# Kernel optimization log

Hardware: AMD Instinct MI355X
Metric: run time of the kernel (lower is better)

The kernel has to match this reference:

```python
import jax, jax.numpy as jnp
import numpy as np

H = 1024      # lstm_hidden_size
LABELS = 122  # slot label size


def setup_inputs() -> dict:
    key = jax.random.key(0)
    ks = jax.random.split(key, 8)
    s_in = 1.0 / np.sqrt(5 * H)
    s_h = 1.0 / np.sqrt(H)
    return {
        "x": jax.random.normal(ks[0], (1, 512, 2 * H), jnp.float32),
        "hi": jax.random.normal(ks[1], (1, 512, 2 * H), jnp.float32),
        # LSTM params (PyTorch layout: gates ordered i, f, g, o)
        "W_ih": jax.random.uniform(ks[2], (4 * H, 5 * H), jnp.float32, -s_in, s_in),
        "W_hh": jax.random.uniform(ks[3], (4 * H, H), jnp.float32, -s_h, s_h),
        "b_ih": jax.random.uniform(ks[4], (4 * H,), jnp.float32, -s_h, s_h),
        "b_hh": jax.random.uniform(ks[5], (4 * H,), jnp.float32, -s_h, s_h),
        "W_fc": jax.random.uniform(ks[6], (LABELS, H), jnp.float32, -s_h, s_h),
        "b_fc": jax.random.uniform(ks[7], (LABELS,), jnp.float32, -s_h, s_h),
    }


def _decode(x, hi, W_ih, W_hh, b_ih, b_hh, W_fc, b_fc):
    # x, hi: [1, L, 2H] -> per-step encoder features [L, 4H] (batch fixed at 1)
    feats = jnp.concatenate([x, hi], axis=-1)[0]
    bias = b_ih + b_hh

    def step(carry, f_t):
        h, c, prev_out = carry
        z = jnp.concatenate([f_t, prev_out])              # [5H]: cat(x_t, hi_t, out_{t-1})
        gates = W_ih @ z + W_hh @ h + bias                # [4H]
        i, f, g, o = jnp.split(gates, 4)
        c_new = jax.nn.sigmoid(f) * c + jax.nn.sigmoid(i) * jnp.tanh(g)
        h_new = jax.nn.sigmoid(o) * jnp.tanh(c_new)
        return (h_new, c_new, h_new), h_new

    zero = jnp.zeros((H,), x.dtype)
    _, outs = jax.lax.scan(step, (zero, zero, zero), feats)  # outs: [L, H]
    res = outs @ W_fc.T + b_fc                               # [L, LABELS]
    return res[None]                                         # [1, L, LABELS]


def reference(x, hi, W_ih, W_hh, b_ih, b_hh, W_fc, b_fc):
    return _decode(x, hi, W_ih, W_hh, b_ih, b_hh, W_fc, b_fc)
```

## Files before the change

kernel.cpp:

```cpp
#include <hip/hip_runtime.h>
#include <hip/hip_fp16.h>
#include <math.h>

#define HD    1024
#define SEQL  512
#define NLAB  122
#define NWG   128
#define TPW   512
#define JPW   8

#define OFF_MSG   ((size_t)0)
#define OFF_HALL  ((size_t)16384)
#define OFF_GATES ((size_t)2113536)
#define OFF_WR    ((size_t)10502144)
#define OFF_W1H   ((size_t)27279360)
#define OFF_FH    ((size_t)60833792)
#define WS_NEED   ((size_t)65028096)
#define REP_MAX   8
#define OFF_MSG8  WS_NEED
#define WS_NEED8  (WS_NEED + (size_t)2 * REP_MAX * HD * 8)

typedef unsigned long long u64;
typedef _Float16 v8h __attribute__((ext_vector_type(8)));
typedef float v4f __attribute__((ext_vector_type(4)));
typedef float v2f __attribute__((ext_vector_type(2)));
typedef unsigned int v4u __attribute__((ext_vector_type(4)));

__global__ __launch_bounds__(256) void prep_wr(const float* __restrict__ W_ih,
                                               const float* __restrict__ W_hh,
                                               float* __restrict__ W_r2) {
    int o = blockIdx.x * 256 + threadIdx.x;
    int g   = o >> 13;
    int i   = (o >> 9) & 15;
    int t   = o & 511;
    int row = t & 31;
    int kq  = t >> 5;
    int gate = row >> 3;
    int jj   = row & 7;
    int R = (gate << 10) + (g << 3) + jj;
    int k = (kq << 6) + (i << 2);
    float4 wa = *(const float4*)(W_ih + (size_t)R * 5120 + 4096 + k);
    float4 wb = *(const float4*)(W_hh + (size_t)R * 1024 + k);
    float4 out;
    out.x = wa.x + wb.x; out.y = wa.y + wb.y; out.z = wa.z + wb.z; out.w = wa.w + wb.w;
    *(float4*)(W_r2 + (size_t)o * 4) = out;
}

static __device__ __forceinline__ uint4 pack8(float4 f0, float4 f1) {
    __half2 p0 = __floats2half2_rn(f0.x, f0.y);
    __half2 p1 = __floats2half2_rn(f0.z, f0.w);
    __half2 p2 = __floats2half2_rn(f1.x, f1.y);
    __half2 p3 = __floats2half2_rn(f1.z, f1.w);
    uint4 o;
    o.x = *(unsigned*)&p0; o.y = *(unsigned*)&p1;
    o.z = *(unsigned*)&p2; o.w = *(unsigned*)&p3;
    return o;
}

__global__ __launch_bounds__(256) void prep_fh(const float* __restrict__ x,
                                               const float* __restrict__ hi,
                                               uint4* __restrict__ F_h) {
    int o = blockIdx.x * 256 + threadIdx.x;
    int t = o >> 9;
    int u = o & 511;
    const float* src = (u < 256) ? (x  + (size_t)t * 2048 + u * 8)
                                 : (hi + (size_t)t * 2048 + (u - 256) * 8);
    F_h[o] = pack8(*(const float4*)src, *(const float4*)(src + 4));
}

__global__ __launch_bounds__(256) void prep_w1h(const float* __restrict__ W_ih,
                                                uint4* __restrict__ W1h) {
    int o = blockIdx.x * 256 + threadIdx.x;
    int r = o >> 9;
    int u = o & 511;
    const float* src = W_ih + (size_t)r * 5120 + u * 8;
    W1h[o] = pack8(*(const float4*)src, *(const float4*)(src + 4));
}

__global__ __launch_bounds__(256) void gates_mfma(const uint4* __restrict__ F_u4,
                                                  const uint4* __restrict__ W_u4,
                                                  const float* __restrict__ b_ih,
                                                  const float* __restrict__ b_hh,
                                                  float* __restrict__ gates_x) {
    __shared__ uint4 AsB[1024];
    const _Float16* Ash = (const _Float16*)AsB;
    const _Float16* Bsh = Ash + 4096;
    const int tid  = threadIdx.x;
    const int wv   = tid >> 6;
    const int lane = tid & 63;
    const int wr   = wv & 1;
    const int wc   = wv >> 1;
    const int n0 = blockIdx.x * 128;
    const int t0 = blockIdx.y * 128;

    const int u0 = tid * 2, u1 = tid * 2 + 1;
    const uint4* aSrc0 = F_u4 + (size_t)(t0 + (u0 >> 2)) * 512 + (u0 & 3);
    const uint4* aSrc1 = F_u4 + (size_t)(t0 + (u1 >> 2)) * 512 + (u1 & 3);
    const uint4* bSrc0 = W_u4 + (size_t)(n0 + (u0 >> 2)) * 512 + (u0 & 3);
    const uint4* bSrc1 = W_u4 + (size_t)(n0 + (u1 >> 2)) * 512 + (u1 & 3);

    v4f acc[4][4];
    #pragma unroll
    for (int mi = 0; mi < 4; ++mi)
        #pragma unroll
        for (int ni = 0; ni < 4; ++ni)
            acc[mi][ni] = (v4f){0.f, 0.f, 0.f, 0.f};

    const int aoff = (wr * 64 + (lane & 15)) * 32 + (lane >> 4) * 8;
    const int boff = (wc * 64 + (lane & 15)) * 32 + (lane >> 4) * 8;

    for (int it = 0; it < 128; ++it) {
        uint4 a0 = aSrc0[it * 4], a1 = aSrc1[it * 4];
        uint4 b0 = bSrc0[it * 4], b1 = bSrc1[it * 4];
        __syncthreads();
        AsB[u0]       = a0; AsB[u1]       = a1;
        AsB[512 + u0] = b0; AsB[512 + u1] = b1;
        __syncthreads();
        v8h a8[4], b8[4];
        #pragma unroll
        for (int mi = 0; mi < 4; ++mi)
            a8[mi] = *(const v8h*)(Ash + aoff + mi * 16 * 32);
        #pragma unroll
        for (int ni = 0; ni < 4; ++ni)
            b8[ni] = *(const v8h*)(Bsh + boff + ni * 16 * 32);
        #pragma unroll
        for (int mi = 0; mi < 4; ++mi)
            #pragma unroll
            for (int ni = 0; ni < 4; ++ni)
                acc[mi][ni] = __builtin_amdgcn_mfma_f32_16x16x32_f16(
                                  a8[mi], b8[ni], acc[mi][ni], 0, 0, 0);
    }

    #pragma unroll
    for (int ni = 0; ni < 4; ++ni) {
        int r = n0 + wc * 64 + ni * 16 + (lane & 15);
        int sidx = ((r & 1023) >> 3) * 32 + (r >> 10) * 8 + (r & 7);
        float bias = b_ih[r] + b_hh[r];
        #pragma unroll
        for (int mi = 0; mi < 4; ++mi) {
            int tb = t0 + wr * 64 + mi * 16 + ((lane >> 4) << 2);
            #pragma unroll
            for (int reg = 0; reg < 4; ++reg)
                gates_x[(size_t)(tb + reg) * 4096 + sidx] = acc[mi][ni][reg] + bias;
        }
    }
}

__global__ __launch_bounds__(256) void gates_gemm_f32(const float* __restrict__ x,
                                                      const float* __restrict__ hi,
                                                      const float* __restrict__ W_ih,
                                                      const float* __restrict__ b_ih,
                                                      const float* __restrict__ b_hh,
                                                      float* __restrict__ gates_x) {
    __shared__ float As[16][68];
    __shared__ float Bs[16][68];
    const int tid = threadIdx.x;
    const int r0 = blockIdx.x * 64;
    const int t0 = blockIdx.y * 64;
    const int tx = tid & 15, ty = tid >> 4;
    const int l   = tid & 63;
    const int kq4 = tid >> 6;

    float acc[4][4] = {};
    for (int kb = 0; kb < 4096; kb += 16) {
        int k = kb + kq4 * 4;
        const float* asrc = (k < 2048) ? (x  + (size_t)(t0 + l) * 2048 + k)
                                       : (hi + (size_t)(t0 + l) * 2048 + (k - 2048));
        float4 a4 = *(const float4*)asrc;
        float4 b4 = *(const float4*)(W_ih + (size_t)(r0 + l) * 5120 + k);
        __syncthreads();
        As[kq4 * 4 + 0][l] = a4.x; As[kq4 * 4 + 1][l] = a4.y;
        As[kq4 * 4 + 2][l] = a4.z; As[kq4 * 4 + 3][l] = a4.w;
        Bs[kq4 * 4 + 0][l] = b4.x; Bs[kq4 * 4 + 1][l] = b4.y;
        Bs[kq4 * 4 + 2][l] = b4.z; Bs[kq4 * 4 + 3][l] = b4.w;
        __syncthreads();
        #pragma unroll
        for (int kk = 0; kk < 16; ++kk) {
            float4 av = *(const float4*)&As[kk][ty * 4];
            float4 bv = *(const float4*)&Bs[kk][tx * 4];
            float a_[4] = {av.x, av.y, av.z, av.w};
            float b_[4] = {bv.x, bv.y, bv.z, bv.w};
            #pragma unroll
            for (int i = 0; i < 4; ++i)
                #pragma unroll
                for (int j = 0; j < 4; ++j)
                    acc[i][j] += a_[i] * b_[j];
        }
    }
    int r = r0 + tx * 4;
    float bias[4];
    #pragma unroll
    for (int j = 0; j < 4; ++j) bias[j] = b_ih[r + j] + b_hh[r + j];
    int gate = r >> 10;
    int g    = (r & 1023) >> 3;
    int jj   = r & 7;
    int sidx = g * 32 + gate * 8 + jj;
    #pragma unroll
    for (int i = 0; i < 4; ++i) {
        float4 o;
        o.x = acc[i][0] + bias[0]; o.y = acc[i][1] + bias[1];
        o.z = acc[i][2] + bias[2]; o.w = acc[i][3] + bias[3];
        *(float4*)(gates_x + (size_t)(t0 + ty * 4 + i) * 4096 + sidx) = o;
    }
}

__global__ __launch_bounds__(512, 1) void lstm_rec(const float* __restrict__ gates_x,
                                                   const float* __restrict__ W_r2,
                                                   float* __restrict__ h_all,
                                                   u64* h_msg, int rep) {
    const int g   = blockIdx.x;
    const int tid = threadIdx.x;
    const int row = tid & 31;
    const int kq  = tid >> 5;
    const int cp  = g & (rep - 1);
    __shared__ float4 W_lds[16][TPW];
    __shared__ float4 h_s4[256];
    __shared__ float  partial[8][36];
    float* h_sf = (float*)h_s4;

    {
        const float4* Wp = (const float4*)W_r2 + (size_t)g * 8192;
        #pragma unroll
        for (int i = 0; i < 16; ++i)
            W_lds[i][tid] = Wp[i * TPW + tid];
    }
    __syncthreads();

    float c = 0.f;
    int budget = 4000000;

    for (int s = 0; s < SEQL; ++s) {
        float gx = 0.f;
        if (tid < 32)
            gx = gates_x[(size_t)s * 4096 + g * 32 + tid];

        asm volatile("" ::: "memory");
        float4 w[16];
        #pragma unroll
        for (int i = 0; i < 16; ++i)
            w[i] = W_lds[i][tid];
        asm volatile("" ::: "memory");

        {
            const u64 addr = (u64)(h_msg +
                                   ((size_t)((s & 1) * rep + cp)) * HD + tid * 2);
            const unsigned want = (unsigned)s;
            v4u ra;
            for (;;) {
                asm volatile(
                    "global_load_dwordx4 %0, %1, off sc1\n\t"
                    "s_waitcnt vmcnt(0)"
                    : "=&v"(ra)
                    : "v"(addr)
                    : "memory");
                if (ra.y == want && ra.w == want) break;
                if (--budget < 0) break;
            }
            ((v2f*)h_sf)[tid] = (v2f){__uint_as_float(ra.x), __uint_as_float(ra.z)};
        }
        asm volatile("" ::: "memory");

        float a0 = 0.f, a1 = 0.f, a2 = 0.f, a3 = 0.f;
        #pragma unroll
        for (int i = 0; i < 16; ++i) {
            float4 h4 = h_s4[kq * 16 + i];
            a0 += w[i].x * h4.x;
            a1 += w[i].y * h4.y;
            a2 += w[i].z * h4.z;
            a3 += w[i].w * h4.w;
        }
        float p = (a0 + a1) + (a2 + a3);
        p += __shfl_xor(p, 32, 64);
        if ((tid & 32) == 0)
            partial[tid >> 6][row] = p;
        __syncthreads();

        if (tid < 32) {
            float sum = gx;
            #pragma unroll
            for (int q = 0; q < 8; ++q) sum += partial[q][tid];
            bool isg = ((tid >> 3) == 2);
            float e   = __expf(isg ? -2.f * sum : -sum);
            float act = isg ? (2.f / (1.f + e) - 1.f) : (1.f / (1.f + e));
            int jj = tid & 7;
            float sf = __shfl(act,  8 + jj, 64);
            float tg = __shfl(act, 16 + jj, 64);
            float so = __shfl(act, 24 + jj, 64);
            if (tid < 8) {
                float si = act;
                c = sf * c + si * tg;
                float th = 2.f / (1.f + __expf(-2.f * c)) - 1.f;
                float h = so * th;
                int j = g * JPW + tid;
                h_all[(size_t)s * HD + j] = h;
                u64 m = ((u64)(unsigned)(s + 1) << 32)
                      | (u64)__float_as_uint(h);
                u64* dst = h_msg + (size_t)(((s + 1) & 1) * rep) * HD + j;
                for (int r = 0; r < rep; ++r)
                    __hip_atomic_store(dst + (size_t)r * HD, m,
                                       __ATOMIC_RELAXED, __HIP_MEMORY_SCOPE_AGENT);
            }
        }
    }
}

__global__ __launch_bounds__(128) void fc_out(const float* __restrict__ h_all,
                                              const float* __restrict__ W_fc,
                                              const float* __restrict__ b_fc,
                                              float* __restrict__ out) {
    const int t0 = blockIdx.x * 4;
    const int tid = threadIdx.x;
    __shared__ float4 h_s[1024];
    const float4* hsrc = (const float4*)(h_all + (size_t)t0 * HD);
    #pragma unroll
    for (int i = 0; i < 8; ++i)
        h_s[tid + i * 128] = hsrc[tid + i * 128];
    __syncthreads();
    if (tid < NLAB) {
        float b = b_fc[tid];
        float acc0 = b, acc1 = b, acc2 = b, acc3 = b;
        const float4* wp = (const float4*)(W_fc + (size_t)tid * HD);
        #pragma unroll 4
        for (int k4 = 0; k4 < 256; ++k4) {
            float4 w = wp[k4];
            float4 h0 = h_s[k4];
            float4 h1 = h_s[256 + k4];
            float4 h2 = h_s[512 + k4];
            float4 h3 = h_s[768 + k4];
            acc0 += w.x*h0.x + w.y*h0.y + w.z*h0.z + w.w*h0.w;
            acc1 += w.x*h1.x + w.y*h1.y + w.z*h1.z + w.w*h1.w;
            acc2 += w.x*h2.x + w.y*h2.y + w.z*h2.z + w.w*h2.w;
            acc3 += w.x*h3.x + w.y*h3.y + w.z*h3.z + w.w*h3.w;
        }
        out[(size_t)(t0 + 0) * NLAB + tid] = acc0;
        out[(size_t)(t0 + 1) * NLAB + tid] = acc1;
        out[(size_t)(t0 + 2) * NLAB + tid] = acc2;
        out[(size_t)(t0 + 3) * NLAB + tid] = acc3;
    }
}

extern "C" void kernel_launch(void* const* d_in, const int* in_sizes, int n_in,
                              void* d_out, int out_size, void* d_ws, size_t ws_size,
                              hipStream_t stream) {
    const float* x    = (const float*)d_in[0];
    const float* hi   = (const float*)d_in[1];
    const float* W_ih = (const float*)d_in[2];
    const float* W_hh = (const float*)d_in[3];
    const float* b_ih = (const float*)d_in[4];
    const float* b_hh = (const float*)d_in[5];
    const float* W_fc = (const float*)d_in[6];
    const float* b_fc = (const float*)d_in[7];
    float* out = (float*)d_out;

    char* ws = (char*)d_ws;
    float* h_all   = (float*)(ws + OFF_HALL);
    float* gates_x = (float*)(ws + OFF_GATES);
    float* W_r2    = (float*)(ws + OFF_WR);
    uint4* W1h     = (uint4*)(ws + OFF_W1H);
    uint4* F_h     = (uint4*)(ws + OFF_FH);

    u64* h_msg;
    int  rep;
    if (ws_size >= WS_NEED8) {
        h_msg = (u64*)(ws + OFF_MSG8);
        rep   = REP_MAX;
        hipMemsetAsync(h_msg, 0, (size_t)2 * REP_MAX * HD * 8, stream);
    } else {
        h_msg = (u64*)(ws + OFF_MSG);
        rep   = 1;
        hipMemsetAsync(h_msg, 0, 16384, stream);
    }

    prep_wr<<<4096, 256, 0, stream>>>(W_ih, W_hh, W_r2);

    if (ws_size >= WS_NEED) {
        prep_fh<<<1024, 256, 0, stream>>>(x, hi, F_h);
        prep_w1h<<<8192, 256, 0, stream>>>(W_ih, W1h);
        dim3 gg(32, 4);
        gates_mfma<<<gg, 256, 0, stream>>>(F_h, W1h, b_ih, b_hh, gates_x);
    } else {
        dim3 gg(64, 8);
        gates_gemm_f32<<<gg, 256, 0, stream>>>(x, hi, W_ih, b_ih, b_hh, gates_x);
    }

    lstm_rec<<<NWG, TPW, 0, stream>>>(gates_x, W_r2, h_all, h_msg, rep);

    fc_out<<<SEQL / 4, 128, 0, stream>>>(h_all, W_fc, b_fc, out);
}
```

Measured before the change: 1.243 ms.

## Fuse input-gate GEMM with LSTM recurrence using per-time-block completion flags

The three prep kernels are merged into one launch. The gates GEMM and the persistent LSTM recurrence now run in a single 256-block kernel: 128 blocks compute GEMM tiles and bump a per-128-step done counter, while the other 128 LSTM blocks wait on that counter before staging 128 steps of gate inputs into LDS. This lets the recurrence start before the whole GEMM finishes and removes a launch boundary. It also drops the replicated h message buffers in favour of a single copy polled with two back-to-back loads. The risks are that the LSTM and GEMM blocks must be co-resident or the spin-wait stalls, and that the GEMM tile shrinks to half width per block.

```diff
diff --git a/kernel.cpp b/kernel.cpp
--- a/kernel.cpp
+++ b/kernel.cpp
@@ -16,9 +16,8 @@
 #define OFF_W1H   ((size_t)27279360)
 #define OFF_FH    ((size_t)60833792)
 #define WS_NEED   ((size_t)65028096)
-#define REP_MAX   8
-#define OFF_MSG8  WS_NEED
-#define WS_NEED8  (WS_NEED + (size_t)2 * REP_MAX * HD * 8)
+#define OFF_DONE  WS_NEED
+#define WS_NEED_F (WS_NEED + 256)
 
 typedef unsigned long long u64;
 typedef _Float16 v8h __attribute__((ext_vector_type(8)));
@@ -26,25 +25,15 @@
 typedef float v2f __attribute__((ext_vector_type(2)));
 typedef unsigned int v4u __attribute__((ext_vector_type(4)));
 
-__global__ __launch_bounds__(256) void prep_wr(const float* __restrict__ W_ih,
-                                               const float* __restrict__ W_hh,
-                                               float* __restrict__ W_r2) {
-    int o = blockIdx.x * 256 + threadIdx.x;
-    int g   = o >> 13;
-    int i   = (o >> 9) & 15;
-    int t   = o & 511;
-    int row = t & 31;
-    int kq  = t >> 5;
-    int gate = row >> 3;
-    int jj   = row & 7;
-    int R = (gate << 10) + (g << 3) + jj;
-    int k = (kq << 6) + (i << 2);
-    float4 wa = *(const float4*)(W_ih + (size_t)R * 5120 + 4096 + k);
-    float4 wb = *(const float4*)(W_hh + (size_t)R * 1024 + k);
-    float4 out;
-    out.x = wa.x + wb.x; out.y = wa.y + wb.y; out.z = wa.z + wb.z; out.w = wa.w + wb.w;
-    *(float4*)(W_r2 + (size_t)o * 4) = out;
-}
+union SMem {
+    struct {
+        float4 W[16][TPW];
+        float4 h4[256];
+        float  part[8][36];
+        float  gxs[4096];
+    } l;
+    uint4 AsB[1024];
+};
 
 static __device__ __forceinline__ uint4 pack8(float4 f0, float4 f1) {
     __half2 p0 = __floats2half2_rn(f0.x, f0.y);
@@ -57,165 +46,134 @@
     return o;
 }
 
-__global__ __launch_bounds__(256) void prep_fh(const float* __restrict__ x,
-                                               const float* __restrict__ hi,
-                                               uint4* __restrict__ F_h) {
-    int o = blockIdx.x * 256 + threadIdx.x;
-    int t = o >> 9;
-    int u = o & 511;
-    const float* src = (u < 256) ? (x  + (size_t)t * 2048 + u * 8)
-                                 : (hi + (size_t)t * 2048 + (u - 256) * 8);
-    F_h[o] = pack8(*(const float4*)src, *(const float4*)(src + 4));
-}
-
-__global__ __launch_bounds__(256) void prep_w1h(const float* __restrict__ W_ih,
+__global__ __launch_bounds__(256) void prep_all(const float* __restrict__ x,
+                                                const float* __restrict__ hi,
+                                                const float* __restrict__ W_ih,
+                                                const float* __restrict__ W_hh,
+                                                float* __restrict__ W_r2,
+                                                uint4* __restrict__ F_h,
                                                 uint4* __restrict__ W1h) {
-    int o = blockIdx.x * 256 + threadIdx.x;
-    int r = o >> 9;
-    int u = o & 511;
-    const float* src = W_ih + (size_t)r * 5120 + u * 8;
-    W1h[o] = pack8(*(const float4*)src, *(const float4*)(src + 4));
-}
-
-__global__ __launch_bounds__(256) void gates_mfma(const uint4* __restrict__ F_u4,
-                                                  const uint4* __restrict__ W_u4,
-                                                  const float* __restrict__ b_ih,
-                                                  const float* __restrict__ b_hh,
-                                                  float* __restrict__ gates_x) {
-    __shared__ uint4 AsB[1024];
+    int b = blockIdx.x;
+    int tid = threadIdx.x;
+    if (b < 4096) {
+        int o = b * 256 + tid;
+        int g   = o >> 13;
+        int i   = (o >> 9) & 15;
+        int t   = o & 511;
+        int row = t & 31;
+        int kq  = t >> 5;
+        int gate = row >> 3;
+        int jj   = row & 7;
+        int R = (gate << 10) + (g << 3) + jj;
+        int k = (kq << 6) + (i << 2);
+        float4 wa = *(const float4*)(W_ih + (size_t)R * 5120 + 4096 + k);
+        float4 wb = *(const float4*)(W_hh + (size_t)R * 1024 + k);
+        float4 out;
+        out.x = wa.x + wb.x; out.y = wa.y + wb.y;
+        out.z = wa.z + wb.z; out.w = wa.w + wb.w;
+        *(float4*)(W_r2 + (size_t)o * 4) = out;
+    } else if (b < 5120) {
+        int o = (b - 4096) * 256 + tid;
+        int t = o >> 9;
+        int u = o & 511;
+        const float* src = (u < 256) ? (x  + (size_t)t * 2048 + u * 8)
+                                     : (hi + (size_t)t * 2048 + (u - 256) * 8);
+        F_h[o] = pack8(*(const float4*)src, *(const float4*)(src + 4));
+    } else {
+        int o = (b - 5120) * 256 + tid;
+        int r = o >> 9;
+        int u = o & 511;
+        const float* src = W_ih + (size_t)r * 5120 + u * 8;
+        W1h[o] = pack8(*(const float4*)src, *(const float4*)(src + 4));
+    }
+}
+
+static __device__ void gates_tile(const uint4* __restrict__ F_u4,
+                                  const uint4* __restrict__ W_u4,
+                                  const float* __restrict__ b_ih,
+                                  const float* __restrict__ b_hh,
+                                  float* __restrict__ gates_x,
+                                  unsigned* __restrict__ done,
+                                  uint4* AsB, int bid, int tid) {
     const _Float16* Ash = (const _Float16*)AsB;
     const _Float16* Bsh = Ash + 4096;
-    const int tid  = threadIdx.x;
     const int wv   = tid >> 6;
     const int lane = tid & 63;
     const int wr   = wv & 1;
     const int wc   = wv >> 1;
-    const int n0 = blockIdx.x * 128;
-    const int t0 = blockIdx.y * 128;
-
-    const int u0 = tid * 2, u1 = tid * 2 + 1;
-    const uint4* aSrc0 = F_u4 + (size_t)(t0 + (u0 >> 2)) * 512 + (u0 & 3);
-    const uint4* aSrc1 = F_u4 + (size_t)(t0 + (u1 >> 2)) * 512 + (u1 & 3);
-    const uint4* bSrc0 = W_u4 + (size_t)(n0 + (u0 >> 2)) * 512 + (u0 & 3);
-    const uint4* bSrc1 = W_u4 + (size_t)(n0 + (u1 >> 2)) * 512 + (u1 & 3);
-
-    v4f acc[4][4];
+    const int n0 = (bid & 31) * 128;
+    const int tb = bid >> 5;
+    const int t0 = tb * 128;
+
+    const int u = tid;
+    const uint4* aSrc = F_u4 + (size_t)(t0 + (u >> 2)) * 512 + (u & 3);
+    const uint4* bSrc = W_u4 + (size_t)(n0 + (u >> 2)) * 512 + (u & 3);
+
+    v4f acc[4][2];
     #pragma unroll
     for (int mi = 0; mi < 4; ++mi)
         #pragma unroll
-        for (int ni = 0; ni < 4; ++ni)
+        for (int ni = 0; ni < 2; ++ni)
             acc[mi][ni] = (v4f){0.f, 0.f, 0.f, 0.f};
 
     const int aoff = (wr * 64 + (lane & 15)) * 32 + (lane >> 4) * 8;
-    const int boff = (wc * 64 + (lane & 15)) * 32 + (lane >> 4) * 8;
+    const int boff = (wc * 32 + (lane & 15)) * 32 + (lane >> 4) * 8;
 
     for (int it = 0; it < 128; ++it) {
-        uint4 a0 = aSrc0[it * 4], a1 = aSrc1[it * 4];
-        uint4 b0 = bSrc0[it * 4], b1 = bSrc1[it * 4];
+        uint4 a = aSrc[it * 4];
+        uint4 b = bSrc[it * 4];
         __syncthreads();
-        AsB[u0]       = a0; AsB[u1]       = a1;
-        AsB[512 + u0] = b0; AsB[512 + u1] = b1;
+        AsB[u]       = a;
+        AsB[512 + u] = b;
         __syncthreads();
-        v8h a8[4], b8[4];
+        v8h a8[4], b8[2];
         #pragma unroll
         for (int mi = 0; mi < 4; ++mi)
             a8[mi] = *(const v8h*)(Ash + aoff + mi * 16 * 32);
         #pragma unroll
-        for (int ni = 0; ni < 4; ++ni)
+        for (int ni = 0; ni < 2; ++ni)
             b8[ni] = *(const v8h*)(Bsh + boff + ni * 16 * 32);
         #pragma unroll
         for (int mi = 0; mi < 4; ++mi)
             #pragma unroll
-            for (int ni = 0; ni < 4; ++ni)
+            for (int ni = 0; ni < 2; ++ni)
                 acc[mi][ni] = __builtin_amdgcn_mfma_f32_16x16x32_f16(
                                   a8[mi], b8[ni], acc[mi][ni], 0, 0, 0);
     }
 
     #pragma unroll
-    for (int ni = 0; ni < 4; ++ni) {
-        int r = n0 + wc * 64 + ni * 16 + (lane & 15);
+    for (int ni = 0; ni < 2; ++ni) {
+        int r = n0 + wc * 32 + ni * 16 + (lane & 15);
         int sidx = ((r & 1023) >> 3) * 32 + (r >> 10) * 8 + (r & 7);
         float bias = b_ih[r] + b_hh[r];
         #pragma unroll
         for (int mi = 0; mi < 4; ++mi) {
-            int tb = t0 + wr * 64 + mi * 16 + ((lane >> 4) << 2);
+            int trow = t0 + wr * 64 + mi * 16 + ((lane >> 4) << 2);
             #pragma unroll
             for (int reg = 0; reg < 4; ++reg)
-                gates_x[(size_t)(tb + reg) * 4096 + sidx] = acc[mi][ni][reg] + bias;
-        }
-    }
-}
-
-__global__ __launch_bounds__(256) void gates_gemm_f32(const float* __restrict__ x,
-                                                      const float* __restrict__ hi,
-                                                      const float* __restrict__ W_ih,
-                                                      const float* __restrict__ b_ih,
-                                                      const float* __restrict__ b_hh,
-                                                      float* __restrict__ gates_x) {
-    __shared__ float As[16][68];
-    __shared__ float Bs[16][68];
-    const int tid = threadIdx.x;
-    const int r0 = blockIdx.x * 64;
-    const int t0 = blockIdx.y * 64;
-    const int tx = tid & 15, ty = tid >> 4;
-    const int l   = tid & 63;
-    const int kq4 = tid >> 6;
-
-    float acc[4][4] = {};
-    for (int kb = 0; kb < 4096; kb += 16) {
-        int k = kb + kq4 * 4;
-        const float* asrc = (k < 2048) ? (x  + (size_t)(t0 + l) * 2048 + k)
-                                       : (hi + (size_t)(t0 + l) * 2048 + (k - 2048));
-        float4 a4 = *(const float4*)asrc;
-        float4 b4 = *(const float4*)(W_ih + (size_t)(r0 + l) * 5120 + k);
-        __syncthreads();
-        As[kq4 * 4 + 0][l] = a4.x; As[kq4 * 4 + 1][l] = a4.y;
-        As[kq4 * 4 + 2][l] = a4.z; As[kq4 * 4 + 3][l] = a4.w;
-        Bs[kq4 * 4 + 0][l] = b4.x; Bs[kq4 * 4 + 1][l] = b4.y;
-        Bs[kq4 * 4 + 2][l] = b4.z; Bs[kq4 * 4 + 3][l] = b4.w;
-        __syncthreads();
-        #pragma unroll
-        for (int kk = 0; kk < 16; ++kk) {
-            float4 av = *(const float4*)&As[kk][ty * 4];
-            float4 bv = *(const float4*)&Bs[kk][tx * 4];
-            float a_[4] = {av.x, av.y, av.z, av.w};
-            float b_[4] = {bv.x, bv.y, bv.z, bv.w};
-            #pragma unroll
-            for (int i = 0; i < 4; ++i)
-                #pragma unroll
-                for (int j = 0; j < 4; ++j)
-                    acc[i][j] += a_[i] * b_[j];
-        }
-    }
-    int r = r0 + tx * 4;
-    float bias[4];
-    #pragma unroll
-    for (int j = 0; j < 4; ++j) bias[j] = b_ih[r + j] + b_hh[r + j];
-    int gate = r >> 10;
-    int g    = (r & 1023) >> 3;
-    int jj   = r & 7;
-    int sidx = g * 32 + gate * 8 + jj;
-    #pragma unroll
-    for (int i = 0; i < 4; ++i) {
-        float4 o;
-        o.x = acc[i][0] + bias[0]; o.y = acc[i][1] + bias[1];
-        o.z = acc[i][2] + bias[2]; o.w = acc[i][3] + bias[3];
-        *(float4*)(gates_x + (size_t)(t0 + ty * 4 + i) * 4096 + sidx) = o;
-    }
-}
-
-__global__ __launch_bounds__(512, 1) void lstm_rec(const float* __restrict__ gates_x,
-                                                   const float* __restrict__ W_r2,
-                                                   float* __restrict__ h_all,
-                                                   u64* h_msg, int rep) {
-    const int g   = blockIdx.x;
-    const int tid = threadIdx.x;
+                __hip_atomic_store(gates_x + (size_t)(trow + reg) * 4096 + sidx,
+                                   acc[mi][ni][reg] + bias,
+                                   __ATOMIC_RELAXED, __HIP_MEMORY_SCOPE_AGENT);
+        }
+    }
+    __syncthreads();
+    if (tid == 0)
+        __hip_atomic_fetch_add(done + tb, 1u,
+                               __ATOMIC_RELEASE, __HIP_MEMORY_SCOPE_AGENT);
+}
+
+static __device__ void lstm_body(const float* __restrict__ gates_x,
+                                 const float* __restrict__ W_r2,
+                                 float* __restrict__ h_all,
+                                 u64* h_msg,
+                                 unsigned* done,
+                                 SMem* sm, int g, int tid) {
     const int row = tid & 31;
     const int kq  = tid >> 5;
-    const int cp  = g & (rep - 1);
-    __shared__ float4 W_lds[16][TPW];
-    __shared__ float4 h_s4[256];
-    __shared__ float  partial[8][36];
+    float4 (*W_lds)[TPW] = sm->l.W;
+    float4* h_s4 = sm->l.h4;
+    float (*partial)[36] = sm->l.part;
+    float* gxs = sm->l.gxs;
     float* h_sf = (float*)h_s4;
 
     {
@@ -230,9 +188,32 @@
     int budget = 4000000;
 
     for (int s = 0; s < SEQL; ++s) {
+        if ((s & 127) == 0) {
+            int tb = s >> 7;
+            if (done) {
+                if (tid == 0) {
+                    int sp = 20000000;
+                    while (__hip_atomic_load(done + tb, __ATOMIC_ACQUIRE,
+                                             __HIP_MEMORY_SCOPE_AGENT) < 32u) {
+                        if (--sp < 0) break;
+                        __builtin_amdgcn_s_sleep(8);
+                    }
+                }
+                __syncthreads();
+            }
+            float4* gxs4 = (float4*)gxs;
+            #pragma unroll
+            for (int k = 0; k < 2; ++k) {
+                int o4 = tid + k * 512;
+                int t  = o4 >> 3, c4 = o4 & 7;
+                gxs4[o4] = *(const float4*)(gates_x + (size_t)(s + t) * 4096
+                                            + g * 32 + c4 * 4);
+            }
+            __syncthreads();
+        }
+
         float gx = 0.f;
-        if (tid < 32)
-            gx = gates_x[(size_t)s * 4096 + g * 32 + tid];
+        if (tid < 32) gx = gxs[(s & 127) * 32 + tid];
 
         asm volatile("" ::: "memory");
         float4 w[16];
@@ -242,19 +223,20 @@
         asm volatile("" ::: "memory");
 
         {
-            const u64 addr = (u64)(h_msg +
-                                   ((size_t)((s & 1) * rep + cp)) * HD + tid * 2);
+            const u64 addr = (u64)(h_msg + (size_t)(s & 1) * HD + tid * 2);
             const unsigned want = (unsigned)s;
-            v4u ra;
+            v4u ra, rb;
             for (;;) {
                 asm volatile(
-                    "global_load_dwordx4 %0, %1, off sc1\n\t"
+                    "global_load_dwordx4 %0, %2, off sc1\n\t"
+                    "global_load_dwordx4 %1, %2, off sc1\n\t"
                     "s_waitcnt vmcnt(0)"
-                    : "=&v"(ra)
+                    : "=&v"(ra), "=&v"(rb)
                     : "v"(addr)
                     : "memory");
                 if (ra.y == want && ra.w == want) break;
-                if (--budget < 0) break;
+                if (rb.y == want && rb.w == want) { ra = rb; break; }
+                if (--budget < 0) { ra = rb; break; }
             }
             ((v2f*)h_sf)[tid] = (v2f){__uint_as_float(ra.x), __uint_as_float(ra.z)};
         }
@@ -295,12 +277,92 @@
                 h_all[(size_t)s * HD + j] = h;
                 u64 m = ((u64)(unsigned)(s + 1) << 32)
                       | (u64)__float_as_uint(h);
-                u64* dst = h_msg + (size_t)(((s + 1) & 1) * rep) * HD + j;
-                for (int r = 0; r < rep; ++r)
-                    __hip_atomic_store(dst + (size_t)r * HD, m,
-                                       __ATOMIC_RELAXED, __HIP_MEMORY_SCOPE_AGENT);
+                __hip_atomic_store(h_msg + (size_t)((s + 1) & 1) * HD + j, m,
+                                   __ATOMIC_RELAXED, __HIP_MEMORY_SCOPE_AGENT);
             }
         }
+    }
+}
+
+__global__ __launch_bounds__(512, 1) void gates_lstm_fused(
+        const uint4* __restrict__ F_u4, const uint4* __restrict__ W_u4,
+        const float* __restrict__ b_ih, const float* __restrict__ b_hh,
+        float* __restrict__ gates_x,
+        const float* __restrict__ W_r2, float* __restrict__ h_all,
+        u64* h_msg, unsigned* done) {
+    __shared__ SMem sm;
+    const int tid = threadIdx.x;
+    if (blockIdx.x < 128)
+        gates_tile(F_u4, W_u4, b_ih, b_hh, gates_x, done, sm.AsB,
+                   blockIdx.x, tid);
+    else
+        lstm_body(gates_x, W_r2, h_all, h_msg, done, &sm,
+                  blockIdx.x - 128, tid);
+}
+
+__global__ __launch_bounds__(512, 1) void lstm_only(
+        const float* __restrict__ gates_x, const float* __restrict__ W_r2,
+        float* __restrict__ h_all, u64* h_msg) {
+    __shared__ SMem sm;
+    lstm_body(gates_x, W_r2, h_all, h_msg, nullptr, &sm,
+              blockIdx.x, threadIdx.x);
+}
+
+__global__ __launch_bounds__(256) void gates_gemm_f32(const float* __restrict__ x,
+                                                      const float* __restrict__ hi,
+                                                      const float* __restrict__ W_ih,
+                                                      const float* __restrict__ b_ih,
+                                                      const float* __restrict__ b_hh,
+                                                      float* __restrict__ gates_x) {
+    __shared__ float As[16][68];
+    __shared__ float Bs[16][68];
+    const int tid = threadIdx.x;
+    const int r0 = blockIdx.x * 64;
+    const int t0 = blockIdx.y * 64;
+    const int tx = tid & 15, ty = tid >> 4;
+    const int l   = tid & 63;
+    const int kq4 = tid >> 6;
+
+    float acc[4][4] = {};
+    for (int kb = 0; kb < 4096; kb += 16) {
+        int k = kb + kq4 * 4;
+        const float* asrc = (k < 2048) ? (x  + (size_t)(t0 + l) * 2048 + k)
+                                       : (hi + (size_t)(t0 + l) * 2048 + (k - 2048));
+        float4 a4 = *(const float4*)asrc;
+        float4 b4 = *(const float4*)(W_ih + (size_t)(r0 + l) * 5120 + k);
+        __syncthreads();
+        As[kq4 * 4 + 0][l] = a4.x; As[kq4 * 4 + 1][l] = a4.y;
+        As[kq4 * 4 + 2][l] = a4.z; As[kq4 * 4 + 3][l] = a4.w;
+        Bs[kq4 * 4 + 0][l] = b4.x; Bs[kq4 * 4 + 1][l] = b4.y;
+        Bs[kq4 * 4 + 2][l] = b4.z; Bs[kq4 * 4 + 3][l] = b4.w;
+        __syncthreads();
+        #pragma unroll
+        for (int kk = 0; kk < 16; ++kk) {
+            float4 av = *(const float4*)&As[kk][ty * 4];
+            float4 bv = *(const float4*)&Bs[kk][tx * 4];
+            float a_[4] = {av.x, av.y, av.z, av.w};
+            float b_[4] = {bv.x, bv.y, bv.z, bv.w};
+            #pragma unroll
+            for (int i = 0; i < 4; ++i)
+                #pragma unroll
+                for (int j = 0; j < 4; ++j)
+                    acc[i][j] += a_[i] * b_[j];
+        }
+    }
+    int r = r0 + tx * 4;
+    float bias[4];
+    #pragma unroll
+    for (int j = 0; j < 4; ++j) bias[j] = b_ih[r + j] + b_hh[r + j];
+    int gate = r >> 10;
+    int g    = (r & 1023) >> 3;
+    int jj   = r & 7;
+    int sidx = g * 32 + gate * 8 + jj;
+    #pragma unroll
+    for (int i = 0; i < 4; ++i) {
+        float4 o;
+        o.x = acc[i][0] + bias[0]; o.y = acc[i][1] + bias[1];
+        o.z = acc[i][2] + bias[2]; o.w = acc[i][3] + bias[3];
+        *(float4*)(gates_x + (size_t)(t0 + ty * 4 + i) * 4096 + sidx) = o;
     }
 }
 
@@ -353,37 +415,27 @@
     float* out = (float*)d_out;
 
     char* ws = (char*)d_ws;
-    float* h_all   = (float*)(ws + OFF_HALL);
-    float* gates_x = (float*)(ws + OFF_GATES);
-    float* W_r2    = (float*)(ws + OFF_WR);
-    uint4* W1h     = (uint4*)(ws + OFF_W1H);
-    uint4* F_h     = (uint4*)(ws + OFF_FH);
-
-    u64* h_msg;
-    int  rep;
-    if (ws_size >= WS_NEED8) {
-        h_msg = (u64*)(ws + OFF_MSG8);
-        rep   = REP_MAX;
-        hipMemsetAsync(h_msg, 0, (size_t)2 * REP_MAX * HD * 8, stream);
+    u64*      h_msg   = (u64*)(ws + OFF_MSG);
+    float*    h_all   = (float*)(ws + OFF_HALL);
+    float*    gates_x = (float*)(ws + OFF_GATES);
+    float*    W_r2    = (float*)(ws + OFF_WR);
+    uint4*    W1h     = (uint4*)(ws + OFF_W1H);
+    uint4*    F_h     = (uint4*)(ws + OFF_FH);
+    unsigned* done    = (unsigned*)(ws + OFF_DONE);
+
+    hipMemsetAsync(h_msg, 0, 16384, stream);
+
+    if (ws_size >= WS_NEED_F) {
+        hipMemsetAsync(done, 0, 256, stream);
+        prep_all<<<13312, 256, 0, stream>>>(x, hi, W_ih, W_hh, W_r2, F_h, W1h);
+        gates_lstm_fused<<<256, TPW, 0, stream>>>(F_h, W1h, b_ih, b_hh, gates_x,
+                                                  W_r2, h_all, h_msg, done);
     } else {
-        h_msg = (u64*)(ws + OFF_MSG);
-        rep   = 1;
-        hipMemsetAsync(h_msg, 0, 16384, stream);
-    }
-
-    prep_wr<<<4096, 256, 0, stream>>>(W_ih, W_hh, W_r2);
-
-    if (ws_size >= WS_NEED) {
-        prep_fh<<<1024, 256, 0, stream>>>(x, hi, F_h);
-        prep_w1h<<<8192, 256, 0, stream>>>(W_ih, W1h);
-        dim3 gg(32, 4);
-        gates_mfma<<<gg, 256, 0, stream>>>(F_h, W1h, b_ih, b_hh, gates_x);
-    } else {
+        prep_all<<<4096, 256, 0, stream>>>(x, hi, W_ih, W_hh, W_r2, F_h, W1h);
         dim3 gg(64, 8);
         gates_gemm_f32<<<gg, 256, 0, stream>>>(x, hi, W_ih, b_ih, b_hh, gates_x);
-    }
-
-    lstm_rec<<<NWG, TPW, 0, stream>>>(gates_x, W_r2, h_all, h_msg, rep);
+        lstm_only<<<NWG, TPW, 0, stream>>>(gates_x, W_r2, h_all, h_msg);
+    }
 
     fc_out<<<SEQL / 4, 128, 0, stream>>>(h_all, W_fc, b_fc, out);
 }
```

Result: slower. 1.341 ms (+8.0%).
